# Kernel optimization log

Hardware: AMD Instinct MI355X
Metric: run time of the kernel (lower is better)

## Reference

```python
import jax, jax.numpy as jnp
from jax import lax
import numpy as np

# Hyperparameters (module defaults)
MIP_K = 31
P_LO, P_HI = 0.01, 0.99
ALPHA = 0.15
MU = 10.0
PD_ITERS = 30
TAU = 0.125
SIG_PD = 0.125
THETA = 1.0
EPS = 1e-6


def _forward_grad(u):
    # forward differences, zero-padded on the far edge -> same shape as u
    dx = jnp.pad(u[..., :, 1:] - u[..., :, :-1], ((0, 0), (0, 0), (0, 0), (0, 1)))
    dy = jnp.pad(u[..., 1:, :] - u[..., :-1, :], ((0, 0), (0, 0), (0, 1), (0, 0)))
    return dx, dy


def _divergence(px, py):
    # backward-difference divergence (adjoint of forward grad)
    div_x = px - jnp.pad(px[..., :, :-1], ((0, 0), (0, 0), (0, 0), (1, 0)))
    div_y = py - jnp.pad(py[..., :-1, :], ((0, 0), (0, 0), (1, 0), (0, 0)))
    return div_x + div_y


def _max_pool(x, k):
    # stride-1 max pool with -inf padding (matches torch F.max_pool2d semantics)
    pad = k // 2
    return lax.reduce_window(
        x, -jnp.inf, lax.max,
        window_dimensions=(1, 1, k, k),
        window_strides=(1, 1, 1, 1),
        padding=((0, 0), (0, 0), (pad, pad), (pad, pad)))


def setup_inputs() -> dict:
    key = jax.random.key(0)
    Iy = jax.random.uniform(key, (16, 3, 512, 512), dtype=jnp.float32)
    return {"Iy": Iy}


def reference(Iy):
    R, G, Bc = Iy[:, 0:1], Iy[:, 1:2], Iy[:, 2:3]

    # MIP coarse depth
    Rmax = _max_pool(R, MIP_K)
    GBmax = jnp.maximum(_max_pool(G, MIP_K), _max_pool(Bc, MIP_K))
    x = jnp.abs(Rmax - GBmax) + R

    # robust per-image percentile normalization to [0,1]
    B = x.shape[0]
    flat = x.reshape(B, -1)
    lo = jnp.quantile(flat, P_LO, axis=1)[:, None, None, None]
    hi = jnp.quantile(flat, P_HI, axis=1)[:, None, None, None]
    N_hat = jnp.clip((x - lo) / (hi - lo + EPS), 0.0, 1.0)

    # fixed edge weights from grad(N_hat), sigma = per-image median grad magnitude
    dxh, dyh = _forward_grad(N_hat)
    grad_mag = jnp.sqrt(dxh * dxh + dyh * dyh + EPS)
    sigma = jnp.maximum(
        jnp.quantile(grad_mag.reshape(B, -1), 0.5, axis=1), EPS)[:, None, None, None]
    Wx = 1.0 + MU * jnp.exp(-jnp.abs(dxh) / sigma)
    Wy = 1.0 + MU * jnp.exp(-jnp.abs(dyh) / sigma)

    # Chambolle-Pock primal-dual iterations for weighted TV-L2
    def step(carry, _):
        u, u_bar, px, py = carry
        dx, dy = _forward_grad(u_bar)
        px = jnp.clip(px + SIG_PD * dx, -ALPHA * Wx, ALPHA * Wx)
        py = jnp.clip(py + SIG_PD * dy, -ALPHA * Wy, ALPHA * Wy)
        v = u + TAU * _divergence(px, py)
        u_new = (v + TAU * N_hat) / (1.0 + TAU)
        u_bar = u_new + THETA * (u_new - u)
        return (u_new, u_bar, px, py), None

    z = jnp.zeros_like(N_hat)
    (u, _, _, _), _ = lax.scan(step, (N_hat, N_hat, z, z), None, length=PD_ITERS)
    return jnp.clip(u, 0.0, 1.0)
```

## Files before the change

### kernel.cpp

```cpp
#include <hip/hip_runtime.h>
#include <math.h>

#define B_ 16
#define W_ 512
#define H_ 512
#define S_ (W_*H_)
#define ALPHA_ 0.15f
#define MU_ 10.0f
#define TAU_ 0.125f
#define SIG_ 0.125f
#define EPS_ 1e-6f
#define INV1PT_ (1.0f/(1.0f+TAU_))
#define NBINS 4096
#define BINSCALE 2048.0f
#define BINW (1.0f/2048.0f)

__global__ __launch_bounds__(256) void hmax_kernel(const float* __restrict__ Iy,
                                                   float* __restrict__ Rh,
                                                   float* __restrict__ GBh){
  __shared__ float bufA[2][544], bufB[2][544];
  int t = threadIdx.x;
  int b = blockIdx.x >> 9;
  int i = blockIdx.x & 511;
  const float* row = Iy + (size_t)b*3*S_ + (size_t)i*W_;
  for (int p = t; p < 544; p += 256){
    int idx = p - 16;
    bool v = (idx >= 0) && (idx < 512);
    bufA[0][p] = v ? row[idx] : -1e30f;
    bufA[1][p] = v ? fmaxf(row[S_+idx], row[2*S_+idx]) : -1e30f;
  }
  __syncthreads();
  float (*src)[544] = bufA; float (*dst)[544] = bufB;
  const int ds[5] = {1, 2, 4, 8, 15};
  #pragma unroll
  for (int sstep = 0; sstep < 5; ++sstep){
    int d = ds[sstep];
    for (int p = t; p < 544; p += 256){
      int q = min(p + d, 543);
      dst[0][p] = fmaxf(src[0][p], src[0][q]);
      dst[1][p] = fmaxf(src[1][p], src[1][q]);
    }
    __syncthreads();
    float (*tmp)[544] = src; src = dst; dst = tmp;
  }
  size_t o = (size_t)b*S_ + (size_t)i*W_;
  for (int p = t; p < 512; p += 256){
    Rh[o+p]  = src[0][p+1];
    GBh[o+p] = src[1][p+1];
  }
}

__global__ __launch_bounds__(256) void vscan_fwd_kernel(const float* __restrict__ Rh,
                                                        const float* __restrict__ GBh,
                                                        float* __restrict__ Rf,
                                                        float* __restrict__ Gf){
  int gid = blockIdx.x*256 + threadIdx.x;
  int col = gid & 8191;
  int c   = gid >> 13;
  int b = col >> 9, j = col & 511;
  int i0 = c*31, i1 = min(i0+31, H_);
  size_t base = (size_t)b*S_ + j;
  float rR = -1e30f, rG = -1e30f;
  for (int i = i0; i < i1; ++i){
    size_t o = base + (size_t)i*W_;
    rR = fmaxf(rR, Rh[o]); rG = fmaxf(rG, GBh[o]);
    Rf[o] = rR; Gf[o] = rG;
  }
}

__global__ __launch_bounds__(256) void vscan_bwd_kernel(const float* __restrict__ Rh,
                                                        const float* __restrict__ GBh,
                                                        const float* __restrict__ Rf,
                                                        const float* __restrict__ Gf,
                                                        const float* __restrict__ Iy,
                                                        float* __restrict__ xo){
  int gid = blockIdx.x*256 + threadIdx.x;
  int col = gid & 8191;
  int c   = gid >> 13;
  int b = col >> 9, j = col & 511;
  int i0 = c*31, i1 = min(i0+31, H_);
  size_t base = (size_t)b*S_ + j;
  const float* IyR = Iy + (size_t)b*3*S_ + j;
  float lR = -1e30f, lG = -1e30f;
  for (int i = i1-1; i >= i0; --i){
    size_t o64 = base + (size_t)i*W_;
    lR = fmaxf(lR, Rh[o64]); lG = fmaxf(lG, GBh[o64]);
    int o = i + 15;
    if (o < H_){
      int bi = min(i + 30, H_-1);
      size_t ob = base + (size_t)bi*W_;
      float mR = fmaxf(lR, Rf[ob]);
      float mG = fmaxf(lG, Gf[ob]);
      xo[base + (size_t)o*W_] = fabsf(mR - mG) + IyR[(size_t)o*W_];
    }
  }
  if (c == 0){
    for (int o = 0; o < 15; ++o){
      size_t ob = base + (size_t)(o+15)*W_;
      float mR = Rf[ob], mG = Gf[ob];
      xo[base + (size_t)o*W_] = fabsf(mR - mG) + IyR[(size_t)o*W_];
    }
  }
}

__global__ __launch_bounds__(256) void hist_build_kernel(const float* __restrict__ data,
                                                         unsigned int* __restrict__ hist){
  __shared__ unsigned int h[NBINS];
  int t = threadIdx.x;
  int b = blockIdx.x >> 4, sub = blockIdx.x & 15;
  for (int p = t; p < NBINS; p += 256) h[p] = 0u;
  __syncthreads();
  const float* p = data + (size_t)b*S_ + (size_t)sub*16384;
  for (int k = 0; k < 64; ++k){
    float x = p[k*256 + t];
    int bin = (int)(x*BINSCALE);
    bin = min(max(bin, 0), NBINS-1);
    atomicAdd(&h[bin], 1u);
  }
  __syncthreads();
  unsigned int* hb = hist + (size_t)(b*16 + sub)*NBINS;
  for (int q = t; q < NBINS; q += 256) hb[q] = h[q];
}

__global__ __launch_bounds__(256) void nhat_gmhist_kernel(const float* __restrict__ xb,
                                                          const float* __restrict__ vx2,
                                                          float* __restrict__ nh,
                                                          unsigned int* __restrict__ hist){
  __shared__ unsigned int h[NBINS];
  int t = threadIdx.x;
  int b = blockIdx.x >> 4, sub = blockIdx.x & 15;
  for (int p = t; p < NBINS; p += 256) h[p] = 0u;
  __syncthreads();
  float lo = vx2[2*b], hi = vx2[2*b+1];
  float inv = 1.0f/(hi - lo + EPS_);
  const float* base = xb + (size_t)b*S_;
  float* nhb = nh + (size_t)b*S_;
  int i0 = sub*16384;
  for (int k = 0; k < 64; ++k){
    int idx = i0 + k*256 + t;
    int row = idx >> 9, col = idx & 511;
    float c = fminf(fmaxf((base[idx] - lo)*inv, 0.f), 1.f);
    float dx = 0.f, dy = 0.f;
    if (col < W_-1) dx = fminf(fmaxf((base[idx+1]  - lo)*inv, 0.f), 1.f) - c;
    if (row < H_-1) dy = fminf(fmaxf((base[idx+W_] - lo)*inv, 0.f), 1.f) - c;
    nhb[idx] = c;
    float g = sqrtf(dx*dx + dy*dy + EPS_);
    int bin = (int)(g*BINSCALE);
    bin = min(max(bin, 0), NBINS-1);
    atomicAdd(&h[bin], 1u);
  }
  __syncthreads();
  unsigned int* hb = hist + (size_t)(b*16 + sub)*NBINS;
  for (int q = t; q < NBINS; q += 256) hb[q] = h[q];
}

__global__ __launch_bounds__(256) void pick_hist_kernel(
    const unsigned int* __restrict__ hist, int r0, int r1, int r2, int r3,
    int nranks, float* __restrict__ outv, int which){
  __shared__ unsigned int part[256];
  __shared__ int s_own[4], s_rem[4];
  __shared__ float s_val[4];
  int t = threadIdx.x, b = blockIdx.x;
  const unsigned int* hb = hist + (size_t)b*16*NBINS;
  unsigned int binc[16];
  #pragma unroll
  for (int k = 0; k < 16; ++k) binc[k] = 0u;
  for (int sub = 0; sub < 16; ++sub){
    const unsigned int* hp = hb + (size_t)sub*NBINS + t*16;
    #pragma unroll
    for (int k = 0; k < 16; ++k) binc[k] += hp[k];
  }
  unsigned int sum = 0u;
  #pragma unroll
  for (int k = 0; k < 16; ++k) sum += binc[k];
  part[t] = sum;
  __syncthreads();
  if (t == 0){
    int rk[4] = {r0, r1, r2, r3};
    for (int ri = 0; ri < nranks; ++ri){
      int rem = rk[ri]; int own = 255;
      for (int q = 0; q < 256; ++q){
        if ((unsigned int)rem < part[q]){ own = q; break; }
        rem -= (int)part[q];
      }
      s_own[ri] = own; s_rem[ri] = rem;
    }
  }
  __syncthreads();
  for (int ri = 0; ri < nranks; ++ri){
    if (t == s_own[ri]){
      int rem = s_rem[ri]; int bin = t*16 + 15;
      #pragma unroll
      for (int q = 0; q < 16; ++q){
        if ((unsigned int)rem < binc[q]){ bin = t*16 + q; break; }
        rem -= (int)binc[q];
      }
      s_val[ri] = ((float)bin + 0.5f) * BINW;
    }
  }
  __syncthreads();
  if (t == 0){
    if (which == 0){
      outv[2*b+0] = s_val[0]*0.57f + s_val[1]*0.43f;
      outv[2*b+1] = s_val[2]*0.43f + s_val[3]*0.57f;
    } else {
      outv[b] = fmaxf(0.5f*(s_val[0] + s_val[1]), EPS_);
    }
  }
}

#define TILE 64
#define CORE 48
#define HALO 8
#define NB 11
#define PSTR 68

#define AW_(d) (ALPHA_*(1.0f + MU_*__expf(-fabsf(d)*invs)))

__global__ __launch_bounds__(1024, 2) void pd_fused_kernel(
    const float* __restrict__ u_in,  const float* __restrict__ ub_in,
    const float* __restrict__ px_in, const float* __restrict__ py_in,
    float* __restrict__ u_out,  float* __restrict__ ub_out,
    float* __restrict__ px_out, float* __restrict__ py_out,
    const float* __restrict__ nh_g, const float* __restrict__ sig_arr,
    int T, int mode)
{
  __shared__ float sA[TILE*PSTR], sB[TILE*PSTR], sP[TILE*PSTR];
  const int t = threadIdx.x;
  const int b = blockIdx.z;
  const int gi0 = blockIdx.y*CORE - HALO;
  const int gj0 = blockIdx.x*CORE - HALO;
  const float invs = 1.0f / sig_arr[b];
  const int pi = t >> 4, pj = t & 15;
  const int c0 = 4*pj;
  const int lane = t & 63;
  const size_t bb = (size_t)b*S_;
  const int gi = gi0 + pi;

  #define STAGE(dst, srcP)                                         \
    _Pragma("unroll")                                              \
    for (int k = 0; k < 4; ++k){                                   \
      int p = t + k*1024; int li = p>>6, lj = p & 63;              \
      int sgi = gi0+li, sgj = gj0+lj;                              \
      int gic_ = min(max(sgi,0),H_-1), gjc_ = min(max(sgj,0),W_-1);\
      dst[li*PSTR+lj] = srcP[bb + (size_t)gic_*W_ + gjc_]; }

  if (mode == 1){ STAGE(sA, nh_g) }
  else          { STAGE(sA, ub_in) }

  const int rD = min(pi+1,TILE-1);
  const int a_o  = pi*PSTR + c0;
  const int a_up = max(pi-1,0)*PSTR + c0;
  const int a_dn = rD*PSTR + c0;

  int gic  = min(max(gi,0),H_-1);
  int gjc4 = min(max(gj0+c0,0), W_-4);
  size_t go = bb + (size_t)gic*W_ + gjc4;
  float nh_r[4], ax[4], ay[4];
  {
    int giD = min(max(min(gi+1, gi0+TILE-1),0),H_-1);
    int gjR = min(max(min(gj0+c0+4, gj0+TILE-1),0),W_-1);
    float4 n0 = *(const float4*)&nh_g[go];
    float4 nD = *(const float4*)&nh_g[bb + (size_t)giD*W_ + gjc4];
    float nR = nh_g[bb + (size_t)gic*W_ + gjR];
    float n0a[4] = {n0.x,n0.y,n0.z,n0.w};
    float nDa[4] = {nD.x,nD.y,nD.z,nD.w};
    #pragma unroll
    for (int c = 0; c < 4; ++c){
      nh_r[c] = n0a[c];
      int gj = gj0 + c0 + c;
      float nhR = (c<3) ? n0a[c+1] : nR;
      bool jb = (gj < 0) || (gj >= W_-1);
      ax[c] = jb ? 0.f : AW_(nhR - n0a[c]);
      ay[c] = (gi < 0 || gi >= H_-1) ? 0.f : AW_(nDa[c] - n0a[c]);
    }
  }

  float u_r[4], px_r[4], py_r[4], ub_r[4];
  if (mode == 1){
    #pragma unroll
    for (int c = 0; c < 4; ++c){
      u_r[c] = nh_r[c]; ub_r[c] = nh_r[c];
      px_r[c] = 0.f; py_r[c] = 0.f;
    }
  } else {
    float4 uv  = *(const float4*)&u_in[go];
    float4 pxv = *(const float4*)&px_in[go];
    float4 pyv = *(const float4*)&py_in[go];
    u_r[0]=uv.x;  u_r[1]=uv.y;  u_r[2]=uv.z;  u_r[3]=uv.w;
    px_r[0]=pxv.x; px_r[1]=pxv.y; px_r[2]=pxv.z; px_r[3]=pxv.w;
    py_r[0]=pyv.x; py_r[1]=pyv.y; py_r[2]=pyv.z; py_r[3]=pyv.w;
  }
  __syncthreads();
  if (mode != 1){
    float4 ubv = *(const float4*)&sA[a_o];
    ub_r[0]=ubv.x; ub_r[1]=ubv.y; ub_r[2]=ubv.z; ub_r[3]=ubv.w;
  }

  for (int s = 0; s < T; ++s){
    float* RB = (s & 1) ? sB : sA;
    float* WB = (s & 1) ? sA : sB;
    float4 dn = *(const float4*)&RB[a_dn];
    float ubL = __shfl(ub_r[3], (lane-1)&63);
    float ubR = __shfl(ub_r[0], (lane+1)&63);
    if (pj == 0)  ubL = ub_r[0];
    if (pj == 15) ubR = ub_r[3];
    (void)ubL;
    float dna[4] = {dn.x,dn.y,dn.z,dn.w};
    #pragma unroll
    for (int c = 0; c < 4; ++c){
      float ubRn = (c<3) ? ub_r[c+1] : ubR;
      px_r[c] = fminf(fmaxf(fmaf(SIG_, ubRn-ub_r[c], px_r[c]), -ax[c]), ax[c]);
      py_r[c] = fminf(fmaxf(fmaf(SIG_, dna[c]-ub_r[c], py_r[c]), -ay[c]), ay[c]);
    }
    *(float4*)&sP[a_o] = make_float4(py_r[0],py_r[1],py_r[2],py_r[3]);
    float pxl3 = __shfl(px_r[3], (lane-1)&63);
    __syncthreads();
    float4 pu = *(const float4*)&sP[a_up];
    float pyu[4] = {pu.x,pu.y,pu.z,pu.w};
    #pragma unroll
    for (int c = 0; c < 4; ++c){
      float pxl = (c>0) ? px_r[c-1] : pxl3;
      float div = px_r[c] + py_r[c] - pxl - pyu[c];
      float un = fmaf(TAU_, div + nh_r[c], u_r[c]) * INV1PT_;
      ub_r[c] = 2.f*un - u_r[c];
      u_r[c] = un;
    }
    if (s < T-1){
      *(float4*)&WB[a_o] = make_float4(ub_r[0],ub_r[1],ub_r[2],ub_r[3]);
      __syncthreads();
    }
  }

  if (pi >= HALO && pi < HALO+CORE && pj >= 2 && pj <= 13 && gi < H_){
    int gj = gj0 + c0;
    if (gj < W_){
      size_t g = bb + (size_t)gi*W_ + gj;
      if (mode == 2){
        *(float4*)&u_out[g] = make_float4(
          fminf(fmaxf(u_r[0],0.f),1.f), fminf(fmaxf(u_r[1],0.f),1.f),
          fminf(fmaxf(u_r[2],0.f),1.f), fminf(fmaxf(u_r[3],0.f),1.f));
      } else {
        *(float4*)&u_out[g]  = make_float4(u_r[0], u_r[1], u_r[2], u_r[3]);
        *(float4*)&ub_out[g] = make_float4(ub_r[0],ub_r[1],ub_r[2],ub_r[3]);
        *(float4*)&px_out[g] = make_float4(px_r[0],px_r[1],px_r[2],px_r[3]);
        *(float4*)&py_out[g] = make_float4(py_r[0],py_r[1],py_r[2],py_r[3]);
      }
    }
  }
}

extern "C" void kernel_launch(void* const* d_in, const int* in_sizes, int n_in,
                              void* d_out, int out_size, void* d_ws, size_t ws_size,
                              hipStream_t stream){
  const float* Iy = (const float*)d_in[0];
  float* out = (float*)d_out;
  char* ws = (char*)d_ws;
  const size_t SLOT = (size_t)B_*S_*sizeof(float);
  float* slot[8];
  for (int q = 0; q < 8; ++q) slot[q] = (float*)(ws + (size_t)q*SLOT);
  float* vx2 = (float*)(ws + (size_t)8*SLOT);
  float* sig = vx2 + 32;

  float* Rh  = slot[0];
  float* GBh = slot[1];
  float* Rf  = slot[5];
  float* Gf  = slot[6];
  float* xb  = slot[2];
  float* nh  = slot[3];
  unsigned int* hist_x  = (unsigned int*)(ws + (size_t)4*SLOT);
  unsigned int* hist_gm = hist_x + (size_t)256*NBINS;

  hmax_kernel<<<B_*H_, 256, 0, stream>>>(Iy, Rh, GBh);
  vscan_fwd_kernel<<<544, 256, 0, stream>>>(Rh, GBh, Rf, Gf);
  vscan_bwd_kernel<<<544, 256, 0, stream>>>(Rh, GBh, Rf, Gf, Iy, xb);
  hist_build_kernel<<<256, 256, 0, stream>>>(xb, hist_x);
  pick_hist_kernel<<<B_, 256, 0, stream>>>(hist_x, 2621, 2622, 259521, 259522, 4, vx2, 0);
  nhat_gmhist_kernel<<<256, 256, 0, stream>>>(xb, vx2, nh, hist_gm);
  pick_hist_kernel<<<B_, 256, 0, stream>>>(hist_gm, 131071, 131072, 0, 0, 2, sig, 1);

  float *uA = slot[1], *ubA = slot[2], *pxA = slot[5], *pyA = slot[6];
  float *uB = slot[0], *ubB = slot[4], *pxB = slot[7], *pyB = out;

  dim3 pdg(NB, NB, B_);
  pd_fused_kernel<<<pdg, 1024, 0, stream>>>(nh, nh, nh, nh,
                                            uA, ubA, pxA, pyA, nh, sig, 8, 1);
  pd_fused_kernel<<<pdg, 1024, 0, stream>>>(uA, ubA, pxA, pyA,
                                            uB, ubB, pxB, pyB, nh, sig, 8, 0);
  pd_fused_kernel<<<pdg, 1024, 0, stream>>>(uB, ubB, pxB, pyB,
                                            uA, ubA, pxA, pyA, nh, sig, 8, 0);
  pd_fused_kernel<<<pdg, 1024, 0, stream>>>(uA, ubA, pxA, pyA,
                                            out, slot[7], slot[7], slot[7], nh, sig, 6, 2);
}
```

Before: 400.3 us.

## Fuse x-histogram into vertical scan and retile PD kernel for fewer launches

The histogram build for the percentile step now happens inside the backward vertical-scan kernel, which removes a separate kernel and a full re-read of x. The histogram partials change to 34 per image, and the pick kernel takes a configurable partial count. The primal-dual tiles now use asymmetric halos (10 rows, 12 columns) so each launch runs 10 steps. That cuts the PD launches from four to three, at the cost of more redundant halo work and a larger grid. Workspace buffers are also reassigned.

```diff
diff --git a/kernel.cpp b/kernel.cpp
--- a/kernel.cpp
+++ b/kernel.cpp
@@ -73,11 +73,17 @@
                                                         const float* __restrict__ Rf,
                                                         const float* __restrict__ Gf,
                                                         const float* __restrict__ Iy,
-                                                        float* __restrict__ xo){
-  int gid = blockIdx.x*256 + threadIdx.x;
+                                                        float* __restrict__ xo,
+                                                        unsigned int* __restrict__ hist){
+  __shared__ unsigned int h[NBINS];
+  int t = threadIdx.x;
+  for (int p = t; p < NBINS; p += 256) h[p] = 0u;
+  __syncthreads();
+  int gid = blockIdx.x*256 + t;
   int col = gid & 8191;
   int c   = gid >> 13;
   int b = col >> 9, j = col & 511;
+  int half = j >> 8;
   int i0 = c*31, i1 = min(i0+31, H_);
   size_t base = (size_t)b*S_ + j;
   const float* IyR = Iy + (size_t)b*3*S_ + j;
@@ -91,34 +97,26 @@
       size_t ob = base + (size_t)bi*W_;
       float mR = fmaxf(lR, Rf[ob]);
       float mG = fmaxf(lG, Gf[ob]);
-      xo[base + (size_t)o*W_] = fabsf(mR - mG) + IyR[(size_t)o*W_];
+      float xv = fabsf(mR - mG) + IyR[(size_t)o*W_];
+      xo[base + (size_t)o*W_] = xv;
+      int bin = (int)(xv*BINSCALE);
+      bin = min(max(bin, 0), NBINS-1);
+      atomicAdd(&h[bin], 1u);
     }
   }
   if (c == 0){
     for (int o = 0; o < 15; ++o){
       size_t ob = base + (size_t)(o+15)*W_;
       float mR = Rf[ob], mG = Gf[ob];
-      xo[base + (size_t)o*W_] = fabsf(mR - mG) + IyR[(size_t)o*W_];
-    }
-  }
-}
-
-__global__ __launch_bounds__(256) void hist_build_kernel(const float* __restrict__ data,
-                                                         unsigned int* __restrict__ hist){
-  __shared__ unsigned int h[NBINS];
-  int t = threadIdx.x;
-  int b = blockIdx.x >> 4, sub = blockIdx.x & 15;
-  for (int p = t; p < NBINS; p += 256) h[p] = 0u;
-  __syncthreads();
-  const float* p = data + (size_t)b*S_ + (size_t)sub*16384;
-  for (int k = 0; k < 64; ++k){
-    float x = p[k*256 + t];
-    int bin = (int)(x*BINSCALE);
-    bin = min(max(bin, 0), NBINS-1);
-    atomicAdd(&h[bin], 1u);
-  }
-  __syncthreads();
-  unsigned int* hb = hist + (size_t)(b*16 + sub)*NBINS;
+      float xv = fabsf(mR - mG) + IyR[(size_t)o*W_];
+      xo[base + (size_t)o*W_] = xv;
+      int bin = (int)(xv*BINSCALE);
+      bin = min(max(bin, 0), NBINS-1);
+      atomicAdd(&h[bin], 1u);
+    }
+  }
+  __syncthreads();
+  unsigned int* hb = hist + (size_t)(b*34 + c*2 + half)*NBINS;
   for (int q = t; q < NBINS; q += 256) hb[q] = h[q];
 }
 
@@ -155,17 +153,18 @@
 }
 
 __global__ __launch_bounds__(256) void pick_hist_kernel(
-    const unsigned int* __restrict__ hist, int r0, int r1, int r2, int r3,
+    const unsigned int* __restrict__ hist, int nsub,
+    int r0, int r1, int r2, int r3,
     int nranks, float* __restrict__ outv, int which){
   __shared__ unsigned int part[256];
   __shared__ int s_own[4], s_rem[4];
   __shared__ float s_val[4];
   int t = threadIdx.x, b = blockIdx.x;
-  const unsigned int* hb = hist + (size_t)b*16*NBINS;
+  const unsigned int* hb = hist + (size_t)b*nsub*NBINS;
   unsigned int binc[16];
   #pragma unroll
   for (int k = 0; k < 16; ++k) binc[k] = 0u;
-  for (int sub = 0; sub < 16; ++sub){
+  for (int sub = 0; sub < nsub; ++sub){
     const unsigned int* hp = hb + (size_t)sub*NBINS + t*16;
     #pragma unroll
     for (int k = 0; k < 16; ++k) binc[k] += hp[k];
@@ -209,10 +208,14 @@
   }
 }
 
-#define TILE 64
-#define CORE 48
-#define HALO 8
-#define NB 11
+#define TY 64
+#define TX 64
+#define HY 10
+#define HX 12
+#define CY 44
+#define CX 40
+#define NBY 12
+#define NBX 13
 #define PSTR 68
 
 #define AW_(d) (ALPHA_*(1.0f + MU_*__expf(-fabsf(d)*invs)))
@@ -225,11 +228,11 @@
     const float* __restrict__ nh_g, const float* __restrict__ sig_arr,
     int T, int mode)
 {
-  __shared__ float sA[TILE*PSTR], sB[TILE*PSTR], sP[TILE*PSTR];
+  __shared__ float sA[TY*PSTR], sB[TY*PSTR], sP[TY*PSTR];
   const int t = threadIdx.x;
   const int b = blockIdx.z;
-  const int gi0 = blockIdx.y*CORE - HALO;
-  const int gj0 = blockIdx.x*CORE - HALO;
+  const int gi0 = blockIdx.y*CY - HY;
+  const int gj0 = blockIdx.x*CX - HX;
   const float invs = 1.0f / sig_arr[b];
   const int pi = t >> 4, pj = t & 15;
   const int c0 = 4*pj;
@@ -248,7 +251,7 @@
   if (mode == 1){ STAGE(sA, nh_g) }
   else          { STAGE(sA, ub_in) }
 
-  const int rD = min(pi+1,TILE-1);
+  const int rD = min(pi+1,TY-1);
   const int a_o  = pi*PSTR + c0;
   const int a_up = max(pi-1,0)*PSTR + c0;
   const int a_dn = rD*PSTR + c0;
@@ -258,8 +261,8 @@
   size_t go = bb + (size_t)gic*W_ + gjc4;
   float nh_r[4], ax[4], ay[4];
   {
-    int giD = min(max(min(gi+1, gi0+TILE-1),0),H_-1);
-    int gjR = min(max(min(gj0+c0+4, gj0+TILE-1),0),W_-1);
+    int giD = min(max(min(gi+1, gi0+TY-1),0),H_-1);
+    int gjR = min(max(min(gj0+c0+4, gj0+TX-1),0),W_-1);
     float4 n0 = *(const float4*)&nh_g[go];
     float4 nD = *(const float4*)&nh_g[bb + (size_t)giD*W_ + gjc4];
     float nR = nh_g[bb + (size_t)gic*W_ + gjR];
@@ -301,11 +304,8 @@
     float* RB = (s & 1) ? sB : sA;
     float* WB = (s & 1) ? sA : sB;
     float4 dn = *(const float4*)&RB[a_dn];
-    float ubL = __shfl(ub_r[3], (lane-1)&63);
     float ubR = __shfl(ub_r[0], (lane+1)&63);
-    if (pj == 0)  ubL = ub_r[0];
     if (pj == 15) ubR = ub_r[3];
-    (void)ubL;
     float dna[4] = {dn.x,dn.y,dn.z,dn.w};
     #pragma unroll
     for (int c = 0; c < 4; ++c){
@@ -332,7 +332,7 @@
     }
   }
 
-  if (pi >= HALO && pi < HALO+CORE && pj >= 2 && pj <= 13 && gi < H_){
+  if (pi >= HY && pi < HY+CY && pj >= 3 && pj <= 12 && gi < H_){
     int gj = gj0 + c0;
     if (gj < W_){
       size_t g = bb + (size_t)gi*W_ + gj;
@@ -368,27 +368,24 @@
   float* Gf  = slot[6];
   float* xb  = slot[2];
   float* nh  = slot[3];
-  unsigned int* hist_x  = (unsigned int*)(ws + (size_t)4*SLOT);
-  unsigned int* hist_gm = hist_x + (size_t)256*NBINS;
+  unsigned int* hist_x  = (unsigned int*)(ws + (size_t)7*SLOT);
+  unsigned int* hist_gm = (unsigned int*)(ws + (size_t)7*SLOT + 9437184);
 
   hmax_kernel<<<B_*H_, 256, 0, stream>>>(Iy, Rh, GBh);
   vscan_fwd_kernel<<<544, 256, 0, stream>>>(Rh, GBh, Rf, Gf);
-  vscan_bwd_kernel<<<544, 256, 0, stream>>>(Rh, GBh, Rf, Gf, Iy, xb);
-  hist_build_kernel<<<256, 256, 0, stream>>>(xb, hist_x);
-  pick_hist_kernel<<<B_, 256, 0, stream>>>(hist_x, 2621, 2622, 259521, 259522, 4, vx2, 0);
+  vscan_bwd_kernel<<<544, 256, 0, stream>>>(Rh, GBh, Rf, Gf, Iy, xb, hist_x);
+  pick_hist_kernel<<<B_, 256, 0, stream>>>(hist_x, 34, 2621, 2622, 259521, 259522, 4, vx2, 0);
   nhat_gmhist_kernel<<<256, 256, 0, stream>>>(xb, vx2, nh, hist_gm);
-  pick_hist_kernel<<<B_, 256, 0, stream>>>(hist_gm, 131071, 131072, 0, 0, 2, sig, 1);
-
-  float *uA = slot[1], *ubA = slot[2], *pxA = slot[5], *pyA = slot[6];
-  float *uB = slot[0], *ubB = slot[4], *pxB = slot[7], *pyB = out;
-
-  dim3 pdg(NB, NB, B_);
+  pick_hist_kernel<<<B_, 256, 0, stream>>>(hist_gm, 16, 131071, 131072, 0, 0, 2, sig, 1);
+
+  float *uA = slot[1], *ubA = out,     *pxA = slot[5], *pyA = slot[6];
+  float *uB = slot[0], *ubB = slot[2], *pxB = slot[7], *pyB = slot[4];
+
+  dim3 pdg(NBX, NBY, B_);
   pd_fused_kernel<<<pdg, 1024, 0, stream>>>(nh, nh, nh, nh,
-                                            uA, ubA, pxA, pyA, nh, sig, 8, 1);
+                                            uA, ubA, pxA, pyA, nh, sig, 10, 1);
   pd_fused_kernel<<<pdg, 1024, 0, stream>>>(uA, ubA, pxA, pyA,
-                                            uB, ubB, pxB, pyB, nh, sig, 8, 0);
+                                            uB, ubB, pxB, pyB, nh, sig, 10, 0);
   pd_fused_kernel<<<pdg, 1024, 0, stream>>>(uB, ubB, pxB, pyB,
-                                            uA, ubA, pxA, pyA, nh, sig, 8, 0);
-  pd_fused_kernel<<<pdg, 1024, 0, stream>>>(uA, ubA, pxA, pyA,
-                                            out, slot[7], slot[7], slot[7], nh, sig, 6, 2);
-}
+                                            out, slot[7], slot[7], slot[7], nh, sig, 10, 2);
+}
```

Result: no change. 401.2 us (+0.2%).
